# Kernel tuning notes

Hardware: AMD Instinct MI355X
Metric: run time of the kernel (lower is better)

## Reference

```python
import jax, jax.numpy as jnp
import numpy as np

NH = 16
HD = 128
ROPE_THETA = 10000.0


def _rope_tables(L, dtype):
    inv_freq = 1.0 / (ROPE_THETA ** (jnp.arange(0, HD, 2, dtype=jnp.float32) / HD))
    t = jnp.arange(L, dtype=jnp.float32)
    freqs = jnp.outer(t, inv_freq)          # [L, HD/2]
    emb = jnp.concatenate([freqs, freqs], axis=-1)  # [L, HD]
    return jnp.cos(emb).astype(dtype), jnp.sin(emb).astype(dtype)


def _rotate_half(x):
    x1, x2 = jnp.split(x, 2, axis=-1)
    return jnp.concatenate([-x2, x1], axis=-1)


def _apply_rope(x, cos, sin):
    return x * cos + _rotate_half(x) * sin


def setup_inputs() -> dict:
    key = jax.random.key(0)
    k1, k2, k3 = jax.random.split(key, 3)
    B, L, H = 2, 2048, 2048
    x = jax.random.normal(k1, (B, L, H), dtype=jnp.float32)
    w_qkv = jax.random.normal(k2, (3 * H, H), dtype=jnp.float32) * 0.02
    w_o = jax.random.normal(k3, (H, H), dtype=jnp.float32) * 0.02
    return {"x": x, "w_qkv": w_qkv, "w_o": w_o}


def reference(x, w_qkv, w_o):
    B, L, H = x.shape
    qkv = x @ w_qkv.T                                   # [B, L, 3H]
    qkv = qkv.reshape(B, L, 3, NH, HD).transpose(2, 0, 3, 1, 4)  # [3, B, NH, L, HD]
    q, k, v = qkv[0], qkv[1], qkv[2]
    cos, sin = _rope_tables(L, x.dtype)
    cos, sin = cos[None, None], sin[None, None]         # [1, 1, L, HD]
    q = _apply_rope(q, cos, sin)
    k = _apply_rope(k, cos, sin)
    scale = 1.0 / jnp.sqrt(jnp.asarray(HD, dtype=x.dtype))
    scores = jnp.einsum('bhqd,bhkd->bhqk', q, k) * scale
    causal = jnp.tril(jnp.ones((L, L), dtype=bool))
    scores = jnp.where(causal[None, None], scores, jnp.asarray(-1e30, dtype=x.dtype))
    attn = jax.nn.softmax(scores, axis=-1)
    out = jnp.einsum('bhqk,bhkd->bhqd', attn, v)        # [B, NH, L, HD]
    out = out.transpose(0, 2, 1, 3).reshape(B, L, H)
    return out @ w_o.T
```

## Files before the change

kernel.cpp:

```cpp
#include <hip/hip_runtime.h>

#define NHEADS 16
#define HD 128
#define LSEQ 2048
#define NBATCH 2
#define HDIM 2048
#define NQKV 6144
#define SCALE 0.08838834764831845f

typedef __attribute__((ext_vector_type(8))) short bfx8;
typedef __attribute__((ext_vector_type(4))) short bfx4;
typedef __attribute__((ext_vector_type(4))) float f32x4;

__device__ __forceinline__ unsigned short f2bf(float x) {
  unsigned u = __float_as_uint(x);
  u += 0x7fffu + ((u >> 16) & 1u);
  return (unsigned short)(u >> 16);
}
__device__ __forceinline__ float bf2f(unsigned short u) {
  return __uint_as_float(((unsigned)u) << 16);
}
__device__ __forceinline__ void gload_lds16(const void* g, void* l) {
  __builtin_amdgcn_global_load_lds(
      (const __attribute__((address_space(1))) unsigned int*)g,
      (__attribute__((address_space(3))) unsigned int*)l, 16, 0, 0);
}

__global__ __launch_bounds__(256) void cast_all_kernel(
    const float* __restrict__ x, const float* __restrict__ wq,
    const float* __restrict__ wo, unsigned short* __restrict__ xb,
    unsigned short* __restrict__ wqb, unsigned short* __restrict__ wob) {
  int i = blockIdx.x * 256 + threadIdx.x;
  const float* in;
  unsigned short* out;
  int li;
  if (i < 2097152) { in = x; out = xb; li = i; }
  else if (i < 2097152 + 3145728) { in = wq; out = wqb; li = i - 2097152; }
  else { in = wo; out = wob; li = i - (2097152 + 3145728); }
  float4 v = ((const float4*)in)[li];
  bfx4 o;
  o[0] = (short)f2bf(v.x);
  o[1] = (short)f2bf(v.y);
  o[2] = (short)f2bf(v.z);
  o[3] = (short)f2bf(v.w);
  ((bfx4*)out)[li] = o;
}

template<int BN, bool BF16OUT>
__global__ __launch_bounds__(512, 4) void gemm128_kernel(
    const unsigned short* __restrict__ A, const unsigned short* __restrict__ B,
    void* __restrict__ Cout, int M, int N, int K) {
  constexpr int NF = BN / 64;
  constexpr int AQ = 2, BQ = BN / 64;
  __shared__ unsigned short lA[2][128 * 64];
  __shared__ unsigned short lB[2][BN * 64];
  const int tid = threadIdx.x;
  const int w = tid >> 6, lane = tid & 63;
  const int g = lane >> 4, ln = lane & 15;
  const int nmt = M >> 7, nnt = N / BN;
  const int nwg = nmt * nnt;
  const int bid = blockIdx.x;
  const int swz = (bid & 7) * (nwg >> 3) + (bid >> 3);
  const int bm = (swz / nnt) * 128, bn = (swz % nnt) * BN;
  const int wm = (w >> 2) * 64;
  const int wn = (w & 3) * (NF * 16);
  const unsigned short* At = A + (size_t)bm * K;
  const unsigned short* Bt = B + (size_t)bn * K;

  auto STG = [&](const unsigned short* src, unsigned short* dst, int q, int k0) {
    int rid = q * 64 + w * 8 + (lane >> 3);
    int slot = lane & 7;
    gload_lds16(src + (size_t)rid * K + k0 + ((slot ^ (rid & 7)) << 3),
                dst + (size_t)(q * 4096 + w * 512));
  };
  auto STAGE_ALL = [&](int buf, int k0) {
#pragma unroll
    for (int q = 0; q < BQ; ++q) STG(Bt, lB[buf], q, k0);
#pragma unroll
    for (int q = 0; q < AQ; ++q) STG(At, lA[buf], q, k0);
  };

  f32x4 acc[4][NF];
#pragma unroll
  for (int i = 0; i < 4; ++i)
#pragma unroll
    for (int j = 0; j < NF; ++j) acc[i][j] = (f32x4){0.f, 0.f, 0.f, 0.f};

  STAGE_ALL(0, 0);
  asm volatile("s_waitcnt vmcnt(0)" ::: "memory");
  __builtin_amdgcn_s_barrier();

  const int nt = K >> 6;
  for (int t = 0; t < nt; ++t) {
    const int cur = t & 1;
    const char* lAc = (const char*)lA[cur];
    const char* lBc = (const char*)lB[cur];
    const bool more = (t + 1 < nt);
    if (more) STAGE_ALL(cur ^ 1, (t + 1) << 6);

    bfx8 bfrag[NF][2];
#pragma unroll
    for (int nf = 0; nf < NF; ++nf)
#pragma unroll
      for (int kk = 0; kk < 2; ++kk)
        bfrag[nf][kk] = *(const bfx8*)(lBc + (wn + nf * 16 + ln) * 128 +
                                       (((kk * 4 + g) ^ (ln & 7)) << 4));
#pragma unroll
    for (int mf = 0; mf < 4; ++mf) {
      bfx8 afrag[2];
#pragma unroll
      for (int kk = 0; kk < 2; ++kk)
        afrag[kk] = *(const bfx8*)(lAc + (wm + mf * 16 + ln) * 128 +
                                   (((kk * 4 + g) ^ (ln & 7)) << 4));
#pragma unroll
      for (int kk = 0; kk < 2; ++kk)
#pragma unroll
        for (int nf = 0; nf < NF; ++nf)
          acc[mf][nf] = __builtin_amdgcn_mfma_f32_16x16x32_bf16(
              afrag[kk], bfrag[nf][kk], acc[mf][nf], 0, 0, 0);
    }

    asm volatile("s_waitcnt vmcnt(0)" ::: "memory");
    __builtin_amdgcn_s_barrier();
  }

#pragma unroll
  for (int mf = 0; mf < 4; ++mf) {
    int row0 = bm + wm + mf * 16 + g * 4;
#pragma unroll
    for (int nf = 0; nf < NF; ++nf) {
      int col = bn + wn + nf * 16 + ln;
#pragma unroll
      for (int r = 0; r < 4; ++r) {
        if constexpr (BF16OUT)
          ((unsigned short*)Cout)[(size_t)(row0 + r) * N + col] = f2bf(acc[mf][nf][r]);
        else
          ((float*)Cout)[(size_t)(row0 + r) * N + col] = acc[mf][nf][r];
      }
    }
  }
}

template<int NF, bool BF16OUT>
__global__ __launch_bounds__(256, 2) void gemm4w_kernel(
    const unsigned short* __restrict__ A, const unsigned short* __restrict__ B,
    void* __restrict__ Cout, int M, int N, int K) {
  constexpr int BN = 2 * NF * 16;
  constexpr int BQ = BN / 32;
  __shared__ unsigned short lA[2][128 * 64];
  __shared__ unsigned short lB[2][BN * 64];
  const int tid = threadIdx.x;
  const int w = tid >> 6, lane = tid & 63;
  const int g = lane >> 4, ln = lane & 15;
  const int nmt = M >> 7, nnt = N / BN;
  const int nwg = nmt * nnt;
  const int bid = blockIdx.x;
  const int swz = (bid & 7) * (nwg >> 3) + (bid >> 3);
  const int bm = (swz / nnt) * 128, bn = (swz % nnt) * BN;
  const int wm = (w >> 1) * 64;
  const int wn = (w & 1) * (NF * 16);
  const unsigned short* At = A + (size_t)bm * K;
  const unsigned short* Bt = B + (size_t)bn * K;

  auto STG = [&](const unsigned short* src, unsigned short* dst, int q, int k0) {
    int rid = q * 32 + w * 8 + (lane >> 3);
    int slot = lane & 7;
    gload_lds16(src + (size_t)rid * K + k0 + ((slot ^ (rid & 7)) << 3),
                dst + (size_t)(q * 2048 + w * 512));
  };
  auto STAGE_ALL = [&](int buf, int k0) {
#pragma unroll
    for (int q = 0; q < BQ; ++q) STG(Bt, lB[buf], q, k0);
#pragma unroll
    for (int q = 0; q < 4; ++q) STG(At, lA[buf], q, k0);
  };

  f32x4 acc[4][NF];
#pragma unroll
  for (int i = 0; i < 4; ++i)
#pragma unroll
    for (int j = 0; j < NF; ++j) acc[i][j] = (f32x4){0.f, 0.f, 0.f, 0.f};

  STAGE_ALL(0, 0);
  asm volatile("s_waitcnt vmcnt(0)" ::: "memory");
  __builtin_amdgcn_s_barrier();

  const int nt = K >> 6;
  for (int t = 0; t < nt; ++t) {
    const int cur = t & 1;
    const char* lAc = (const char*)lA[cur];
    const char* lBc = (const char*)lB[cur];
    const bool more = (t + 1 < nt);
    if (more) STAGE_ALL(cur ^ 1, (t + 1) << 6);

    bfx8 bfrag[NF][2];
#pragma unroll
    for (int nf = 0; nf < NF; ++nf)
#pragma unroll
      for (int kk = 0; kk < 2; ++kk)
        bfrag[nf][kk] = *(const bfx8*)(lBc + (wn + nf * 16 + ln) * 128 +
                                       (((kk * 4 + g) ^ (ln & 7)) << 4));
#pragma unroll
    for (int mf = 0; mf < 4; ++mf) {
      bfx8 afrag[2];
#pragma unroll
      for (int kk = 0; kk < 2; ++kk)
        afrag[kk] = *(const bfx8*)(lAc + (wm + mf * 16 + ln) * 128 +
                                   (((kk * 4 + g) ^ (ln & 7)) << 4));
#pragma unroll
      for (int kk = 0; kk < 2; ++kk)
#pragma unroll
        for (int nf = 0; nf < NF; ++nf)
          acc[mf][nf] = __builtin_amdgcn_mfma_f32_16x16x32_bf16(
              afrag[kk], bfrag[nf][kk], acc[mf][nf], 0, 0, 0);
    }

    asm volatile("s_waitcnt vmcnt(0)" ::: "memory");
    __builtin_amdgcn_s_barrier();
  }

#pragma unroll
  for (int mf = 0; mf < 4; ++mf) {
    int row0 = bm + wm + mf * 16 + g * 4;
#pragma unroll
    for (int nf = 0; nf < NF; ++nf) {
      int col = bn + wn + nf * 16 + ln;
#pragma unroll
      for (int r = 0; r < 4; ++r) {
        if constexpr (BF16OUT)
          ((unsigned short*)Cout)[(size_t)(row0 + r) * N + col] = f2bf(acc[mf][nf][r]);
        else
          ((float*)Cout)[(size_t)(row0 + r) * N + col] = acc[mf][nf][r];
      }
    }
  }
}

__global__ __launch_bounds__(256) void rope_scatter_kernel(
    const unsigned short* __restrict__ qkv,
    unsigned short* __restrict__ Qo, unsigned short* __restrict__ Ko,
    unsigned short* __restrict__ Vt) {
  __shared__ unsigned short lV[32 * 128];
  const int bh = blockIdx.x;
  const int l0 = blockIdx.y * 32;
  const int b = bh >> 4, h = bh & 15;
  const int tid = threadIdx.x;
#pragma unroll
  for (int it = 0; it < 2; ++it) {
    int idx = it * 256 + tid;
    int ll = idx >> 4;
    int dq = idx & 15;
    int l = l0 + ll;
    const unsigned short* row = qkv + (size_t)(b * LSEQ + l) * NQKV + h * HD;
    bfx4 qlo = *(const bfx4*)(row + dq * 4);
    bfx4 qhi = *(const bfx4*)(row + 64 + dq * 4);
    bfx4 klo = *(const bfx4*)(row + 2048 + dq * 4);
    bfx4 khi = *(const bfx4*)(row + 2048 + 64 + dq * 4);
    bfx4 vlo = *(const bfx4*)(row + 4096 + dq * 4);
    bfx4 vhi = *(const bfx4*)(row + 4096 + 64 + dq * 4);
    bfx4 oqlo, oqhi, oklo, okhi;
#pragma unroll
    for (int e = 0; e < 4; ++e) {
      int d2 = dq * 4 + e;
      float invf = exp2f(-(float)d2 * 0.2076205059304601f);
      float fr = (float)l * invf;
      float s, c;
      sincosf(fr, &s, &c);
      float xq1 = bf2f((unsigned short)qlo[e]), xq2 = bf2f((unsigned short)qhi[e]);
      oqlo[e] = (short)f2bf(xq1 * c - xq2 * s);
      oqhi[e] = (short)f2bf(xq2 * c + xq1 * s);
      float xk1 = bf2f((unsigned short)klo[e]), xk2 = bf2f((unsigned short)khi[e]);
      oklo[e] = (short)f2bf(xk1 * c - xk2 * s);
      okhi[e] = (short)f2bf(xk2 * c + xk1 * s);
    }
    size_t obase = ((size_t)bh * LSEQ + l) * HD;
    *(bfx4*)(Qo + obase + dq * 4) = oqlo;
    *(bfx4*)(Qo + obase + 64 + dq * 4) = oqhi;
    *(bfx4*)(Ko + obase + dq * 4) = oklo;
    *(bfx4*)(Ko + obase + 64 + dq * 4) = okhi;
    *(bfx4*)(lV + ll * 128 + dq * 4) = vlo;
    *(bfx4*)(lV + ll * 128 + 64 + dq * 4) = vhi;
  }
  __syncthreads();
#pragma unroll
  for (int it = 0; it < 16; ++it) {
    int idx = it * 256 + tid;
    int d = idx >> 5;
    int ll = idx & 31;
    Vt[((size_t)bh * HD + d) * LSEQ + l0 + ll] = lV[ll * 128 + d];
  }
}

__global__ __launch_bounds__(512, 4) void flash_kernel(
    const unsigned short* __restrict__ Q, const unsigned short* __restrict__ K,
    const unsigned short* __restrict__ Vt, unsigned short* __restrict__ O) {
  __shared__ unsigned short lKs[2][64 * 128];
  __shared__ unsigned short lVs[2][128 * 64];
  __shared__ unsigned short lP[8][16 * 40];
  const int bh = blockIdx.x;
  const int qy = (int)blockIdx.y;
  const int qt = (qy < 8) ? (15 - qy) : (qy - 8);
  const int q0 = qt * 128;
  const int tid = threadIdx.x;
  const int w = tid >> 6, lane = tid & 63;
  const int g = lane >> 4, ln = lane & 15;
  const int q0w = q0 + w * 16;
  const unsigned short* Qb = Q + (size_t)bh * LSEQ * HD;
  const unsigned short* Kb = K + (size_t)bh * LSEQ * HD;
  const unsigned short* Vb = Vt + (size_t)bh * HD * LSEQ;
  unsigned short* Pw = lP[w];

  auto STAGE = [&](int buf, int kv0s) {
#pragma unroll
    for (int s = 0; s < 2; ++s) {
      int rl = s * 32 + w * 4 + (lane >> 4);
      int slot = lane & 15;
      const unsigned short* src =
          Kb + (size_t)(kv0s + rl) * HD + ((slot ^ (rl & 15)) * 8);
      gload_lds16(src, &lKs[buf][(s * 8192 + w * 1024) / 2]);
    }
#pragma unroll
    for (int s = 0; s < 2; ++s) {
      int d = s * 64 + w * 8 + (lane >> 3);
      int slot = lane & 7;
      const unsigned short* src =
          Vb + (size_t)d * LSEQ + kv0s + ((slot ^ (d & 7)) * 8);
      gload_lds16(src, &lVs[buf][(s * 8192 + w * 1024) / 2]);
    }
  };

  bfx8 qf[4];
#pragma unroll
  for (int c = 0; c < 4; ++c)
    qf[c] = *(const bfx8*)(Qb + (size_t)(q0w + ln) * HD + c * 32 + g * 8);

  f32x4 o[8];
#pragma unroll
  for (int dt = 0; dt < 8; ++dt) o[dt] = (f32x4){0.f, 0.f, 0.f, 0.f};
  float m = -1e30f, sum = 0.f;
  const int qg = q0w + ln;
  const int nch = 2 * qt + 2;

  STAGE(0, 0);
  __syncthreads();

  for (int ch = 0; ch < nch; ++ch) {
    const int kv0 = ch * 64;
    const int cur = ch & 1;
    if (ch + 1 < nch) STAGE(cur ^ 1, kv0 + 64);

    if (kv0 <= q0w + 15) {
      const char* lK0 = (const char*)lKs[cur];
      const char* lV0 = (const char*)lVs[cur];
      f32x4 s4[4];
#pragma unroll
      for (int kt = 0; kt < 4; ++kt) s4[kt] = (f32x4){0.f, 0.f, 0.f, 0.f};
      __builtin_amdgcn_s_setprio(1);
#pragma unroll
      for (int c = 0; c < 4; ++c) {
        const int cbb = c * 64 + g * 16;
#pragma unroll
        for (int kt = 0; kt < 4; ++kt) {
          bfx8 kf = *(const bfx8*)(lK0 + (kt * 16 + ln) * 256 + (cbb ^ (ln << 4)));
          s4[kt] = __builtin_amdgcn_mfma_f32_16x16x32_bf16(kf, qf[c], s4[kt], 0, 0, 0);
        }
      }
      __builtin_amdgcn_s_setprio(0);
      float tm = -1e30f;
      if (kv0 + 63 <= q0w) {
#pragma unroll
        for (int kt = 0; kt < 4; ++kt)
#pragma unroll
          for (int r = 0; r < 4; ++r) {
            s4[kt][r] *= SCALE;
            tm = fmaxf(tm, s4[kt][r]);
          }
      } else {
#pragma unroll
        for (int kt = 0; kt < 4; ++kt)
#pragma unroll
          for (int r = 0; r < 4; ++r) {
            int kvr = kv0 + kt * 16 + 4 * g + r;
            float v = (kvr <= qg) ? s4[kt][r] * SCALE : -1e30f;
            s4[kt][r] = v;
            tm = fmaxf(tm, v);
          }
      }
      tm = fmaxf(tm, __shfl_xor(tm, 16));
      tm = fmaxf(tm, __shfl_xor(tm, 32));
      float f = 1.f;
      const bool dorescale = !__all(tm <= m + 8.f);
      if (dorescale) {
        float mnew = fmaxf(m, tm);
        f = __expf(m - mnew);
        m = mnew;
      }
      float ts = 0.f;
      bfx4 pb4[4];
#pragma unroll
      for (int kt = 0; kt < 4; ++kt)
#pragma unroll
        for (int r = 0; r < 4; ++r) {
          float p = __expf(s4[kt][r] - m);
          ts += p;
          pb4[kt][r] = (short)f2bf(p);
        }
      ts += __shfl_xor(ts, 16);
      ts += __shfl_xor(ts, 32);
      sum = sum * f + ts;
      float fr0 = 1.f, fr1 = 1.f, fr2 = 1.f, fr3 = 1.f;
      if (dorescale) {
        fr0 = __shfl(f, 4 * g + 0);
        fr1 = __shfl(f, 4 * g + 1);
        fr2 = __shfl(f, 4 * g + 2);
        fr3 = __shfl(f, 4 * g + 3);
      }
#pragma unroll
      for (int kvh = 0; kvh < 2; ++kvh) {
        asm volatile("s_waitcnt lgkmcnt(0)" ::: "memory");
        __builtin_amdgcn_sched_barrier(0);
        *(bfx4*)(Pw + ln * 40 + 4 * g) = pb4[2 * kvh];
        *(bfx4*)(Pw + ln * 40 + 16 + 4 * g) = pb4[2 * kvh + 1];
        asm volatile("s_waitcnt lgkmcnt(0)" ::: "memory");
        __builtin_amdgcn_sched_barrier(0);
        bfx8 pf = *(const bfx8*)(Pw + ln * 40 + g * 8);
        if (kvh == 0 && dorescale) {
#pragma unroll
          for (int dt = 0; dt < 8; ++dt) {
            o[dt][0] *= fr0; o[dt][1] *= fr1; o[dt][2] *= fr2; o[dt][3] *= fr3;
          }
        }
        __builtin_amdgcn_s_setprio(1);
#pragma unroll
        for (int dt = 0; dt < 8; ++dt) {
          bfx8 vf = *(const bfx8*)(lV0 + (dt * 16 + ln) * 128 +
                                   ((kvh * 64 + g * 16) ^ ((ln & 7) << 4)));
          o[dt] = __builtin_amdgcn_mfma_f32_16x16x32_bf16(pf, vf, o[dt], 0, 0, 0);
        }
        __builtin_amdgcn_s_setprio(0);
      }
    }
    __syncthreads();
  }

  float inv = 1.f / sum;
  float ir0 = __shfl(inv, 4 * g + 0);
  float ir1 = __shfl(inv, 4 * g + 1);
  float ir2 = __shfl(inv, 4 * g + 2);
  float ir3 = __shfl(inv, 4 * g + 3);
  const int b = bh >> 4, h = bh & 15;
  unsigned short* Ob = O + (size_t)b * LSEQ * HDIM + h * HD;
#pragma unroll
  for (int dt = 0; dt < 8; ++dt) {
    Ob[(size_t)(q0w + 4 * g + 0) * HDIM + dt * 16 + ln] = f2bf(o[dt][0] * ir0);
    Ob[(size_t)(q0w + 4 * g + 1) * HDIM + dt * 16 + ln] = f2bf(o[dt][1] * ir1);
    Ob[(size_t)(q0w + 4 * g + 2) * HDIM + dt * 16 + ln] = f2bf(o[dt][2] * ir2);
    Ob[(size_t)(q0w + 4 * g + 3) * HDIM + dt * 16 + ln] = f2bf(o[dt][3] * ir3);
  }
}

extern "C" void kernel_launch(void* const* d_in, const int* in_sizes, int n_in,
                              void* d_out, int out_size, void* d_ws, size_t ws_size,
                              hipStream_t stream) {
  const float* x = (const float*)d_in[0];
  const float* w_qkv = (const float*)d_in[1];
  const float* w_o = (const float*)d_in[2];
  float* out = (float*)d_out;
  char* ws = (char*)d_ws;

  unsigned short* xb    = (unsigned short*)(ws + 0);
  unsigned short* wqkvb = (unsigned short*)(ws + 16777216);
  unsigned short* wob   = (unsigned short*)(ws + 41943040);
  unsigned short* qkvb  = (unsigned short*)(ws + 50331648);
  unsigned short* qb    = (unsigned short*)(ws + 100663296);
  unsigned short* kb    = (unsigned short*)(ws + 117440512);
  unsigned short* vtb   = (unsigned short*)(ws + 134217728);
  unsigned short* attnb = (unsigned short*)(ws + 0);

  cast_all_kernel<<<24576, 256, 0, stream>>>(x, w_qkv, w_o, xb, wqkvb, wob);

  gemm128_kernel<192, true><<<(4096 / 128) * (6144 / 192), 512, 0, stream>>>(
      xb, wqkvb, (void*)qkvb, 4096, 6144, 2048);

  rope_scatter_kernel<<<dim3(32, 64), 256, 0, stream>>>(qkvb, qb, kb, vtb);

  flash_kernel<<<dim3(32, 16), 512, 0, stream>>>(qb, kb, vtb, attnb);

  gemm4w_kernel<4, false><<<(4096 / 128) * (2048 / 128), 256, 0, stream>>>(
      attnb, wob, (void*)out, 4096, 2048, 2048);
}
```

Before: 263.6 us.

## Fuse RoPE and Q/K/V scatter into QKV GEMM epilogue via permuted weights

Result: no change. 262.6 us (-0.4%).

```diff
diff --git a/kernel.cpp b/kernel.cpp
--- a/kernel.cpp
+++ b/kernel.cpp
@@ -33,37 +33,62 @@
   int i = blockIdx.x * 256 + threadIdx.x;
   const float* in;
   unsigned short* out;
-  int li;
-  if (i < 2097152) { in = x; out = xb; li = i; }
-  else if (i < 2097152 + 3145728) { in = wq; out = wqb; li = i - 2097152; }
-  else { in = wo; out = wob; li = i - (2097152 + 3145728); }
+  int li, lo;
+  if (i < 2097152) {
+    in = x; out = xb; li = i; lo = i;
+  } else if (i < 2097152 + 3145728) {
+    in = wq; out = wqb; li = i - 2097152;
+    int r = li >> 9, c4 = li & 511;
+    int seg = r >> 11, within = r & 2047;
+    int h = within >> 7, dd = within & 127;
+    int d2 = dd & 63, hi = dd >> 6;
+    int pos = ((d2 >> 3) << 4) | (d2 & 7) | (hi << 3);
+    lo = (((seg << 11) + (h << 7) + pos) << 9) + c4;
+  } else {
+    in = wo; out = wob; li = i - (2097152 + 3145728);
+    int n = li >> 9, c4 = li & 511;
+    int k0 = c4 << 2;
+    int h = k0 >> 7, dd = k0 & 127;
+    int d2 = dd & 63, hi = dd >> 6;
+    int pos = ((d2 >> 3) << 4) | (d2 & 7) | (hi << 3);
+    lo = (n << 9) + (h << 5) + (pos >> 2);
+  }
   float4 v = ((const float4*)in)[li];
   bfx4 o;
   o[0] = (short)f2bf(v.x);
   o[1] = (short)f2bf(v.y);
   o[2] = (short)f2bf(v.z);
   o[3] = (short)f2bf(v.w);
-  ((bfx4*)out)[li] = o;
-}
-
-template<int BN, bool BF16OUT>
-__global__ __launch_bounds__(512, 4) void gemm128_kernel(
+  ((bfx4*)out)[lo] = o;
+}
+
+__global__ __launch_bounds__(256) void table_kernel(float2* __restrict__ tbl) {
+  int idx = blockIdx.x * 256 + threadIdx.x;
+  int l = idx >> 6, d2 = idx & 63;
+  float invf = exp2f(-(float)d2 * 0.2076205059304601f);
+  float s, c;
+  sincosf((float)l * invf, &s, &c);
+  tbl[idx] = (float2){c, s};
+}
+
+__global__ __launch_bounds__(512, 4) void gemm_qkv_kernel(
     const unsigned short* __restrict__ A, const unsigned short* __restrict__ B,
-    void* __restrict__ Cout, int M, int N, int K) {
-  constexpr int NF = BN / 64;
-  constexpr int AQ = 2, BQ = BN / 64;
-  __shared__ unsigned short lA[2][128 * 64];
-  __shared__ unsigned short lB[2][BN * 64];
+    unsigned short* __restrict__ Qo, unsigned short* __restrict__ Ko,
+    unsigned short* __restrict__ Vt, const float2* __restrict__ tbl) {
+  constexpr int K = 2048, BN = 192, NF = 3;
+  __shared__ unsigned short smem[(128 + BN) * 64 * 2];
+  unsigned short* lA0 = smem;
+  unsigned short* lB0 = smem + 2 * 128 * 64;
   const int tid = threadIdx.x;
   const int w = tid >> 6, lane = tid & 63;
   const int g = lane >> 4, ln = lane & 15;
-  const int nmt = M >> 7, nnt = N / BN;
-  const int nwg = nmt * nnt;
+  const int nnt = 32;
+  const int nwg = 32 * 32;
   const int bid = blockIdx.x;
   const int swz = (bid & 7) * (nwg >> 3) + (bid >> 3);
   const int bm = (swz / nnt) * 128, bn = (swz % nnt) * BN;
   const int wm = (w >> 2) * 64;
-  const int wn = (w & 3) * (NF * 16);
+  const int wn = (w & 3) * 48;
   const unsigned short* At = A + (size_t)bm * K;
   const unsigned short* Bt = B + (size_t)bn * K;
 
@@ -75,9 +100,9 @@
   };
   auto STAGE_ALL = [&](int buf, int k0) {
 #pragma unroll
-    for (int q = 0; q < BQ; ++q) STG(Bt, lB[buf], q, k0);
-#pragma unroll
-    for (int q = 0; q < AQ; ++q) STG(At, lA[buf], q, k0);
+    for (int q = 0; q < 3; ++q) STG(Bt, lB0 + buf * (BN * 64), q, k0);
+#pragma unroll
+    for (int q = 0; q < 2; ++q) STG(At, lA0 + buf * (128 * 64), q, k0);
   };
 
   f32x4 acc[4][NF];
@@ -93,8 +118,8 @@
   const int nt = K >> 6;
   for (int t = 0; t < nt; ++t) {
     const int cur = t & 1;
-    const char* lAc = (const char*)lA[cur];
-    const char* lBc = (const char*)lB[cur];
+    const char* lAc = (const char*)(lA0 + cur * (128 * 64));
+    const char* lBc = (const char*)(lB0 + cur * (BN * 64));
     const bool more = (t + 1 < nt);
     if (more) STAGE_ALL(cur ^ 1, (t + 1) << 6);
 
@@ -124,19 +149,50 @@
     __builtin_amdgcn_s_barrier();
   }
 
-#pragma unroll
-  for (int mf = 0; mf < 4; ++mf) {
-    int row0 = bm + wm + mf * 16 + g * 4;
-#pragma unroll
-    for (int nf = 0; nf < NF; ++nf) {
-      int col = bn + wn + nf * 16 + ln;
-#pragma unroll
-      for (int r = 0; r < 4; ++r) {
-        if constexpr (BF16OUT)
-          ((unsigned short*)Cout)[(size_t)(row0 + r) * N + col] = f2bf(acc[mf][nf][r]);
-        else
-          ((float*)Cout)[(size_t)(row0 + r) * N + col] = acc[mf][nf][r];
-      }
+  const bool hasV = (bn + BN > 4096);
+#pragma unroll
+  for (int nf = 0; nf < NF; ++nf) {
+    int cb = bn + wn + nf * 16;
+    int seg = cb >> 11;
+    int gcol = cb + ln;
+    if (seg < 2) {
+      int h = (gcol & 2047) >> 7;
+      int pdd = gcol & 127;
+      int d2 = ((pdd >> 4) << 3) | (pdd & 7);
+      float sgn = (pdd & 8) ? 1.f : -1.f;
+      unsigned short* dst = (seg == 0) ? Qo : Ko;
+#pragma unroll
+      for (int mf = 0; mf < 4; ++mf)
+#pragma unroll
+        for (int r = 0; r < 4; ++r) {
+          int row = bm + wm + mf * 16 + g * 4 + r;
+          int bb = row >> 11, l = row & 2047;
+          float2 cs = tbl[(l << 6) + d2];
+          float v = acc[mf][nf][r];
+          float p = __shfl_xor(v, 8);
+          float o = v * cs.x + sgn * p * cs.y;
+          dst[(((size_t)((bb << 4) + h) * 2048 + l) << 7) + pdd] = f2bf(o);
+        }
+    } else {
+      int c = wn + nf * 16 + ln;
+#pragma unroll
+      for (int mf = 0; mf < 4; ++mf)
+#pragma unroll
+        for (int r = 0; r < 4; ++r)
+          smem[c * 136 + (wm + mf * 16 + g * 4 + r)] = f2bf(acc[mf][nf][r]);
+    }
+  }
+  if (hasV) {
+    __syncthreads();
+    int cs0 = (bn < 4096) ? (4096 - bn) : 0;
+    int nV = BN - cs0;
+    int bb = bm >> 11, l0 = bm & 2047;
+    for (int idx = tid; idx < nV * 16; idx += 512) {
+      int c = cs0 + (idx >> 4), part = idx & 15;
+      int gcol = bn + c;
+      int h = (gcol & 2047) >> 7, pdd = gcol & 127;
+      bfx8 vv = *(const bfx8*)(smem + c * 136 + part * 8);
+      *(bfx8*)(Vt + (((size_t)((bb << 4) + h) << 7) + pdd) * 2048 + l0 + part * 8) = vv;
     }
   }
 }
@@ -236,61 +292,6 @@
   }
 }
 
-__global__ __launch_bounds__(256) void rope_scatter_kernel(
-    const unsigned short* __restrict__ qkv,
-    unsigned short* __restrict__ Qo, unsigned short* __restrict__ Ko,
-    unsigned short* __restrict__ Vt) {
-  __shared__ unsigned short lV[32 * 128];
-  const int bh = blockIdx.x;
-  const int l0 = blockIdx.y * 32;
-  const int b = bh >> 4, h = bh & 15;
-  const int tid = threadIdx.x;
-#pragma unroll
-  for (int it = 0; it < 2; ++it) {
-    int idx = it * 256 + tid;
-    int ll = idx >> 4;
-    int dq = idx & 15;
-    int l = l0 + ll;
-    const unsigned short* row = qkv + (size_t)(b * LSEQ + l) * NQKV + h * HD;
-    bfx4 qlo = *(const bfx4*)(row + dq * 4);
-    bfx4 qhi = *(const bfx4*)(row + 64 + dq * 4);
-    bfx4 klo = *(const bfx4*)(row + 2048 + dq * 4);
-    bfx4 khi = *(const bfx4*)(row + 2048 + 64 + dq * 4);
-    bfx4 vlo = *(const bfx4*)(row + 4096 + dq * 4);
-    bfx4 vhi = *(const bfx4*)(row + 4096 + 64 + dq * 4);
-    bfx4 oqlo, oqhi, oklo, okhi;
-#pragma unroll
-    for (int e = 0; e < 4; ++e) {
-      int d2 = dq * 4 + e;
-      float invf = exp2f(-(float)d2 * 0.2076205059304601f);
-      float fr = (float)l * invf;
-      float s, c;
-      sincosf(fr, &s, &c);
-      float xq1 = bf2f((unsigned short)qlo[e]), xq2 = bf2f((unsigned short)qhi[e]);
-      oqlo[e] = (short)f2bf(xq1 * c - xq2 * s);
-      oqhi[e] = (short)f2bf(xq2 * c + xq1 * s);
-      float xk1 = bf2f((unsigned short)klo[e]), xk2 = bf2f((unsigned short)khi[e]);
-      oklo[e] = (short)f2bf(xk1 * c - xk2 * s);
-      okhi[e] = (short)f2bf(xk2 * c + xk1 * s);
-    }
-    size_t obase = ((size_t)bh * LSEQ + l) * HD;
-    *(bfx4*)(Qo + obase + dq * 4) = oqlo;
-    *(bfx4*)(Qo + obase + 64 + dq * 4) = oqhi;
-    *(bfx4*)(Ko + obase + dq * 4) = oklo;
-    *(bfx4*)(Ko + obase + 64 + dq * 4) = okhi;
-    *(bfx4*)(lV + ll * 128 + dq * 4) = vlo;
-    *(bfx4*)(lV + ll * 128 + 64 + dq * 4) = vhi;
-  }
-  __syncthreads();
-#pragma unroll
-  for (int it = 0; it < 16; ++it) {
-    int idx = it * 256 + tid;
-    int d = idx >> 5;
-    int ll = idx & 31;
-    Vt[((size_t)bh * HD + d) * LSEQ + l0 + ll] = lV[ll * 128 + d];
-  }
-}
-
 __global__ __launch_bounds__(512, 4) void flash_kernel(
     const unsigned short* __restrict__ Q, const unsigned short* __restrict__ K,
     const unsigned short* __restrict__ Vt, unsigned short* __restrict__ O) {
@@ -471,18 +472,16 @@
   unsigned short* xb    = (unsigned short*)(ws + 0);
   unsigned short* wqkvb = (unsigned short*)(ws + 16777216);
   unsigned short* wob   = (unsigned short*)(ws + 41943040);
-  unsigned short* qkvb  = (unsigned short*)(ws + 50331648);
   unsigned short* qb    = (unsigned short*)(ws + 100663296);
   unsigned short* kb    = (unsigned short*)(ws + 117440512);
   unsigned short* vtb   = (unsigned short*)(ws + 134217728);
+  float2* tbl           = (float2*)(ws + 150994944);
   unsigned short* attnb = (unsigned short*)(ws + 0);
 
   cast_all_kernel<<<24576, 256, 0, stream>>>(x, w_qkv, w_o, xb, wqkvb, wob);
-
-  gemm128_kernel<192, true><<<(4096 / 128) * (6144 / 192), 512, 0, stream>>>(
-      xb, wqkvb, (void*)qkvb, 4096, 6144, 2048);
-
-  rope_scatter_kernel<<<dim3(32, 64), 256, 0, stream>>>(qkvb, qb, kb, vtb);
+  table_kernel<<<512, 256, 0, stream>>>(tbl);
+
+  gemm_qkv_kernel<<<1024, 512, 0, stream>>>(xb, wqkvb, qb, kb, vtb, tbl);
 
   flash_kernel<<<dim3(32, 16), 512, 0, stream>>>(qb, kb, vtb, attnb);
 
```
